# Performance work log

Measured on AMD Instinct MI355X. Metric: run time of the kernel, lower is better.

Reference implementation:

```python
import jax, jax.numpy as jnp
import numpy as np
import math

N_ANGLES = 8
HIGH_FREQ_RATIO = 0.3


def setup_inputs() -> dict:
    key = jax.random.key(0)
    k1, k2 = jax.random.split(key)
    x = jax.random.normal(k1, (4, 256, 256, 256), dtype=jnp.float32)
    # learnable per-angle weights, init near enhance_init=1.0 with small perturbation
    angle_weights = 1.0 + 0.1 * jax.random.normal(k2, (N_ANGLES,), dtype=jnp.float32)
    return {"x": x, "angle_weights": angle_weights}


def _angle_gain(H, W, angle_weights):
    # Build [H, W] real gain: angle-sector weight in the high-frequency band, 1 elsewhere.
    cy, cx = H // 2, W // 2
    y = jnp.arange(H, dtype=jnp.float32)[:, None] - cy
    x = jnp.arange(W, dtype=jnp.float32)[None, :] - cx
    r = jnp.sqrt(y * y + x * x)
    theta = jnp.arctan2(y, x) + math.pi  # [0, 2*pi]
    angle_step = 2.0 * math.pi / N_ANGLES
    angle_idx = jnp.mod(jnp.floor(theta / angle_step).astype(jnp.int32), N_ANGLES)
    r_max = min(cy, cx)
    high_freq_mask = r > HIGH_FREQ_RATIO * r_max
    weights = angle_weights[angle_idx]  # [H, W]
    return jnp.where(high_freq_mask, weights, jnp.ones_like(weights))


def reference(x, angle_weights):
    # x: [B, C, H, W]
    H, W = x.shape[-2], x.shape[-1]
    gain = _angle_gain(H, W, angle_weights)  # [H, W], real
    xf = jnp.fft.fftshift(jnp.fft.fft2(x, norm="ortho"), axes=(-2, -1))
    # mag*gain * exp(i*phase) == gain * (mag*exp(i*phase)) == gain * spectrum (gain real)
    xf_enh = xf * gain
    x_enh = jnp.fft.ifft2(jnp.fft.ifftshift(xf_enh, axes=(-2, -1)), norm="ortho").real
    return x + x_enh
```

## Files before the change

### kernel.cpp

```cpp
#include <hip/hip_runtime.h>
#include <math.h>

#define PI_F 3.14159265358979323846f
#define WSYNC() asm volatile("s_waitcnt lgkmcnt(0)" ::: "memory")

__device__ __forceinline__ float2 cmul(float2 a, float2 b) {
    return make_float2(a.x * b.x - a.y * b.y, a.x * b.y + a.y * b.x);
}
__device__ __forceinline__ float2 cmulc(float2 a, float2 b) {
    return make_float2(a.x * b.x + a.y * b.y, a.y * b.x - a.x * b.y);
}
__device__ __forceinline__ int digitrev4(int p) {
    return ((p & 3) << 6) | (((p >> 2) & 3) << 4) | (((p >> 4) & 3) << 2) | ((p >> 6) & 3);
}
__device__ __forceinline__ int SW(int i) { return i ^ ((i >> 4) & 15); }

__device__ __forceinline__ void tw3(int eu, float2& w1, float2& w2, float2& w3) {
    float sn, cs;
    __sincosf(-(2.0f * PI_F / 256.0f) * (float)eu, &sn, &cs);
    w1 = make_float2(cs, sn);
    w2 = cmul(w1, w1);
    w3 = cmul(w2, w1);
}

__device__ __forceinline__ void bfly4_fwd(float2 a0, float2 a1, float2 a2, float2 a3,
                                          float2& o0, float2& o1, float2& o2, float2& o3) {
    float2 t0 = make_float2(a0.x + a2.x, a0.y + a2.y);
    float2 t1 = make_float2(a0.x - a2.x, a0.y - a2.y);
    float2 t2 = make_float2(a1.x + a3.x, a1.y + a3.y);
    float2 u  = make_float2(a1.x - a3.x, a1.y - a3.y);
    float2 t3 = make_float2(u.y, -u.x);
    o0 = make_float2(t0.x + t2.x, t0.y + t2.y);
    o1 = make_float2(t1.x + t3.x, t1.y + t3.y);
    o2 = make_float2(t0.x - t2.x, t0.y - t2.y);
    o3 = make_float2(t1.x - t3.x, t1.y - t3.y);
}
__device__ __forceinline__ void bfly4_inv(float2 a0, float2 a1, float2 a2, float2 a3,
                                          float2& o0, float2& o1, float2& o2, float2& o3) {
    float2 t0 = make_float2(a0.x + a2.x, a0.y + a2.y);
    float2 t1 = make_float2(a0.x - a2.x, a0.y - a2.y);
    float2 t2 = make_float2(a1.x + a3.x, a1.y + a3.y);
    float2 u  = make_float2(a1.x - a3.x, a1.y - a3.y);
    float2 t3 = make_float2(-u.y, u.x);
    o0 = make_float2(t0.x + t2.x, t0.y + t2.y);
    o1 = make_float2(t1.x + t3.x, t1.y + t3.y);
    o2 = make_float2(t0.x - t2.x, t0.y - t2.y);
    o3 = make_float2(t1.x - t3.x, t1.y - t3.y);
}

template<int S>
__device__ __forceinline__ void stage_fwd_j(float2* line, int j, float2 w1, float2 w2, float2 w3) {
    const int h = 1 << (2 * S);
    int k  = j & (h - 1);
    int i0 = ((j >> (2 * S)) << (2 * S + 2)) + k;
    int p0 = SW(i0), p1 = SW(i0 + h), p2 = SW(i0 + 2 * h), p3 = SW(i0 + 3 * h);
    float2 a0 = line[p0], a1 = line[p1], a2 = line[p2], a3 = line[p3];
    float2 o0, o1, o2, o3;
    bfly4_fwd(a0, a1, a2, a3, o0, o1, o2, o3);
    line[p0] = o0;
    line[p1] = cmul(o1, w1);
    line[p2] = cmul(o2, w2);
    line[p3] = cmul(o3, w3);
}
template<int S>
__device__ __forceinline__ void stage_inv_j(float2* line, int j, float2 w1, float2 w2, float2 w3) {
    const int h = 1 << (2 * S);
    int k  = j & (h - 1);
    int i0 = ((j >> (2 * S)) << (2 * S + 2)) + k;
    int p0 = SW(i0), p1 = SW(i0 + h), p2 = SW(i0 + 2 * h), p3 = SW(i0 + 3 * h);
    float2 b0 = line[p0];
    float2 b1 = cmulc(line[p1], w1);
    float2 b2 = cmulc(line[p2], w2);
    float2 b3 = cmulc(line[p3], w3);
    float2 o0, o1, o2, o3;
    bfly4_inv(b0, b1, b2, b3, o0, o1, o2, o3);
    line[p0] = o0; line[p1] = o1; line[p2] = o2; line[p3] = o3;
}

__device__ __forceinline__ float gain1(float fy, float fx, const float* sw) {
    float r2 = fy * fy + fx * fx;
    float theta = atan2f(fy, fx) + PI_F;
    int idx = ((int)floorf(theta * (4.0f / PI_F))) & 7;
    float wv = sw[idx];
    return (r2 > 1474.56f) ? wv : 1.0f;
}

__global__ __launch_bounds__(256) void k_gain_lut(const float* __restrict__ wts, float* __restrict__ lut2) {
    __shared__ float sw[8];
    int h = threadIdx.x, w = blockIdx.x;
    if (h < 8) sw[h] = wts[h];
    __syncthreads();
    int kw = digitrev4(w), kh = digitrev4(h);
    float fx  = (kw < 128) ? (float)kw : (float)(kw - 256);
    float fx2 = (kw == 128) ? -128.0f : -fx;
    float fy  = (kh < 128) ? (float)kh : (float)(kh - 256);
    float fy2 = (kh == 128) ? -128.0f : -fy;
    float g1 = gain1(fy, fx, sw);
    float g2 = gain1(fy2, fx2, sw);
    lut2[w * 256 + h] = (1.0f + 0.5f * (g1 + g2)) * (1.0f / 65536.0f);
}

__global__ __launch_bounds__(256) void k_row_fwd(const float* __restrict__ x, float* __restrict__ out) {
    __shared__ float2 lds[8][256];
    int t = threadIdx.x, wv = t >> 6, lane = t & 63;
    int gr = blockIdx.x * 8 + wv * 2;
    int q = gr >> 8, h = gr & 255;
    int plane = ((q >> 7) << 8) + ((q & 127) << 1);
    size_t rA = ((size_t)plane << 16) + ((size_t)h << 8);
    size_t rB = rA + 65536;
    float2* L0 = lds[wv * 2];
    float2* L1 = lds[wv * 2 + 1];
    int w = lane * 4;
    float4 re0 = *(const float4*)(x + rA + w);
    float4 im0 = *(const float4*)(x + rB + w);
    float4 re1 = *(const float4*)(x + rA + 256 + w);
    float4 im1 = *(const float4*)(x + rB + 256 + w);
    float2 w31, w32, w33, w21, w22, w23, w11, w12, w13;
    tw3(lane,             w31, w32, w33);
    tw3((lane & 15) << 2, w21, w22, w23);
    tw3((lane & 3)  << 4, w11, w12, w13);
    int s0 = SW(w), s1 = SW(w + 1), s2 = SW(w + 2), s3 = SW(w + 3);
    L0[s0] = make_float2(re0.x, im0.x); L0[s1] = make_float2(re0.y, im0.y);
    L0[s2] = make_float2(re0.z, im0.z); L0[s3] = make_float2(re0.w, im0.w);
    L1[s0] = make_float2(re1.x, im1.x); L1[s1] = make_float2(re1.y, im1.y);
    L1[s2] = make_float2(re1.z, im1.z); L1[s3] = make_float2(re1.w, im1.w);
    WSYNC();
    stage_fwd_j<3>(L0, lane, w31, w32, w33); stage_fwd_j<3>(L1, lane, w31, w32, w33); WSYNC();
    stage_fwd_j<2>(L0, lane, w21, w22, w23); stage_fwd_j<2>(L1, lane, w21, w22, w23); WSYNC();
    stage_fwd_j<1>(L0, lane, w11, w12, w13); stage_fwd_j<1>(L1, lane, w11, w12, w13); WSYNC();
    {
        float2 o0, o1, o2, o3;
        bfly4_fwd(L0[s0], L0[s1], L0[s2], L0[s3], o0, o1, o2, o3);
        *(float4*)(out + rA + w) = make_float4(o0.x, o1.x, o2.x, o3.x);
        *(float4*)(out + rB + w) = make_float4(o0.y, o1.y, o2.y, o3.y);
        bfly4_fwd(L1[s0], L1[s1], L1[s2], L1[s3], o0, o1, o2, o3);
        *(float4*)(out + rA + 256 + w) = make_float4(o0.x, o1.x, o2.x, o3.x);
        *(float4*)(out + rB + 256 + w) = make_float4(o0.y, o1.y, o2.y, o3.y);
    }
}

template<bool USE_LUT>
__global__ __launch_bounds__(256) void k_col(float* __restrict__ data,
                                             const float* __restrict__ lut2,
                                             const float* __restrict__ wts) {
    __shared__ float2 tile[16][256];
    int t = threadIdx.x;
    int q = blockIdx.x >> 4, wt = blockIdx.x & 15, w0 = wt * 16;
    int plane = ((q >> 7) << 8) + ((q & 127) << 1);
    size_t baseA = ((size_t)plane << 16) + (size_t)w0;
    size_t baseB = baseA + 65536;
    int c0 = (t & 3) * 4, h0 = (t >> 2) * 4;
    int wv = t >> 6, lane = t & 63;
    int i0 = lane * 4;

    float4 gAr[2], gBr[2];
    if (!USE_LUT) {
        if (t < 8) ((float*)tile)[t] = wts[t];
        __syncthreads();
        const float* swp = (const float*)tile;
#pragma unroll
        for (int cp = 0; cp < 2; ++cp) {
#pragma unroll
            for (int cc = 0; cc < 2; ++cc) {
                int col = wv * 4 + cp * 2 + cc;
                int kw = digitrev4(w0 + col);
                float fx  = (kw < 128) ? (float)kw : (float)(kw - 256);
                float fx2 = (kw == 128) ? -128.0f : -fx;
                float4 g;
#pragma unroll
                for (int d = 0; d < 4; ++d) {
                    int kh = digitrev4(i0 + d);
                    float fy  = (kh < 128) ? (float)kh : (float)(kh - 256);
                    float fy2 = (kh == 128) ? -128.0f : -fy;
                    float g1v = gain1(fy, fx, swp);
                    float g2v = gain1(fy2, fx2, swp);
                    (&g.x)[d] = (1.0f + 0.5f * (g1v + g2v)) * (1.0f / 65536.0f);
                }
                if (cc == 0) gAr[cp] = g; else gBr[cp] = g;
            }
        }
        __syncthreads();
    }

    {
        float4 reR[4], imR[4];
#pragma unroll
        for (int r = 0; r < 4; ++r) {
            reR[r] = *(const float4*)(data + baseA + (size_t)(h0 + r) * 256 + c0);
            imR[r] = *(const float4*)(data + baseB + (size_t)(h0 + r) * 256 + c0);
        }
#pragma unroll
        for (int r = 0; r < 4; ++r) {
            int p = SW(h0 + r);
#pragma unroll
            for (int k = 0; k < 4; ++k)
                tile[c0 + k][p] = make_float2((&reR[r].x)[k], (&imR[r].x)[k]);
        }
    }
    __syncthreads();

    float2 w31, w32, w33, w21, w22, w23, w11, w12, w13;
    tw3(lane,             w31, w32, w33);
    tw3((lane & 15) << 2, w21, w22, w23);
    tw3((lane & 3)  << 4, w11, w12, w13);
    int p0 = SW(i0), p1 = SW(i0 + 1), p2 = SW(i0 + 2), p3 = SW(i0 + 3);
#pragma unroll
    for (int cp = 0; cp < 2; ++cp) {
        int colA = wv * 4 + cp * 2, colB = colA + 1;
        float2* LA = tile[colA];
        float2* LB = tile[colB];
        float4 gA, gB;
        if (USE_LUT) {
            gA = *(const float4*)(lut2 + (size_t)(w0 + colA) * 256 + i0);
            gB = *(const float4*)(lut2 + (size_t)(w0 + colB) * 256 + i0);
        } else {
            gA = gAr[cp]; gB = gBr[cp];
        }
        stage_fwd_j<3>(LA, lane, w31, w32, w33); stage_fwd_j<3>(LB, lane, w31, w32, w33); WSYNC();
        stage_fwd_j<2>(LA, lane, w21, w22, w23); stage_fwd_j<2>(LB, lane, w21, w22, w23); WSYNC();
        stage_fwd_j<1>(LA, lane, w11, w12, w13); stage_fwd_j<1>(LB, lane, w11, w12, w13); WSYNC();
        {
            float2 o0, o1, o2, o3, r0, r1, r2, r3;
            bfly4_fwd(LA[p0], LA[p1], LA[p2], LA[p3], o0, o1, o2, o3);
            o0.x *= gA.x; o0.y *= gA.x; o1.x *= gA.y; o1.y *= gA.y;
            o2.x *= gA.z; o2.y *= gA.z; o3.x *= gA.w; o3.y *= gA.w;
            bfly4_inv(o0, o1, o2, o3, r0, r1, r2, r3);
            LA[p0] = r0; LA[p1] = r1; LA[p2] = r2; LA[p3] = r3;
            bfly4_fwd(LB[p0], LB[p1], LB[p2], LB[p3], o0, o1, o2, o3);
            o0.x *= gB.x; o0.y *= gB.x; o1.x *= gB.y; o1.y *= gB.y;
            o2.x *= gB.z; o2.y *= gB.z; o3.x *= gB.w; o3.y *= gB.w;
            bfly4_inv(o0, o1, o2, o3, r0, r1, r2, r3);
            LB[p0] = r0; LB[p1] = r1; LB[p2] = r2; LB[p3] = r3;
        }
        WSYNC();
        stage_inv_j<1>(LA, lane, w11, w12, w13); stage_inv_j<1>(LB, lane, w11, w12, w13); WSYNC();
        stage_inv_j<2>(LA, lane, w21, w22, w23); stage_inv_j<2>(LB, lane, w21, w22, w23); WSYNC();
        stage_inv_j<3>(LA, lane, w31, w32, w33); stage_inv_j<3>(LB, lane, w31, w32, w33); WSYNC();
    }
    __syncthreads();

    {
#pragma unroll
        for (int r = 0; r < 4; ++r) {
            int p = SW(h0 + r);
            float2 v0 = tile[c0 + 0][p], v1 = tile[c0 + 1][p];
            float2 v2 = tile[c0 + 2][p], v3 = tile[c0 + 3][p];
            *(float4*)(data + baseA + (size_t)(h0 + r) * 256 + c0) = make_float4(v0.x, v1.x, v2.x, v3.x);
            *(float4*)(data + baseB + (size_t)(h0 + r) * 256 + c0) = make_float4(v0.y, v1.y, v2.y, v3.y);
        }
    }
}

__global__ __launch_bounds__(256) void k_row_inv(float* __restrict__ data) {
    __shared__ float2 lds[8][256];
    int t = threadIdx.x, wv = t >> 6, lane = t & 63;
    int gr = blockIdx.x * 8 + wv * 2;
    int q = gr >> 8, h = gr & 255;
    int plane = ((q >> 7) << 8) + ((q & 127) << 1);
    size_t rA = ((size_t)plane << 16) + ((size_t)h << 8);
    size_t rB = rA + 65536;
    float2* L0 = lds[wv * 2];
    float2* L1 = lds[wv * 2 + 1];
    int w = lane * 4;
    float4 re0 = *(const float4*)(data + rA + w);
    float4 im0 = *(const float4*)(data + rB + w);
    float4 re1 = *(const float4*)(data + rA + 256 + w);
    float4 im1 = *(const float4*)(data + rB + 256 + w);
    float2 w31, w32, w33, w21, w22, w23, w11, w12, w13;
    tw3(lane,             w31, w32, w33);
    tw3((lane & 15) << 2, w21, w22, w23);
    tw3((lane & 3)  << 4, w11, w12, w13);
    int s0 = SW(w), s1 = SW(w + 1), s2 = SW(w + 2), s3 = SW(w + 3);
    {
        float2 o0, o1, o2, o3;
        bfly4_inv(make_float2(re0.x, im0.x), make_float2(re0.y, im0.y),
                  make_float2(re0.z, im0.z), make_float2(re0.w, im0.w), o0, o1, o2, o3);
        L0[s0] = o0; L0[s1] = o1; L0[s2] = o2; L0[s3] = o3;
        bfly4_inv(make_float2(re1.x, im1.x), make_float2(re1.y, im1.y),
                  make_float2(re1.z, im1.z), make_float2(re1.w, im1.w), o0, o1, o2, o3);
        L1[s0] = o0; L1[s1] = o1; L1[s2] = o2; L1[s3] = o3;
    }
    WSYNC();
    stage_inv_j<1>(L0, lane, w11, w12, w13); stage_inv_j<1>(L1, lane, w11, w12, w13); WSYNC();
    stage_inv_j<2>(L0, lane, w21, w22, w23); stage_inv_j<2>(L1, lane, w21, w22, w23); WSYNC();
    stage_inv_j<3>(L0, lane, w31, w32, w33); stage_inv_j<3>(L1, lane, w31, w32, w33); WSYNC();
    float2 a0 = L0[s0], a1 = L0[s1], a2 = L0[s2], a3 = L0[s3];
    float2 b0 = L1[s0], b1 = L1[s1], b2 = L1[s2], b3 = L1[s3];
    *(float4*)(data + rA + w)       = make_float4(a0.x, a1.x, a2.x, a3.x);
    *(float4*)(data + rB + w)       = make_float4(a0.y, a1.y, a2.y, a3.y);
    *(float4*)(data + rA + 256 + w) = make_float4(b0.x, b1.x, b2.x, b3.x);
    *(float4*)(data + rB + 256 + w) = make_float4(b0.y, b1.y, b2.y, b3.y);
}

extern "C" void kernel_launch(void* const* d_in, const int* in_sizes, int n_in,
                              void* d_out, int out_size, void* d_ws, size_t ws_size,
                              hipStream_t stream) {
    const float* x   = (const float*)d_in[0];
    const float* wts = (const float*)d_in[1];
    float* out = (float*)d_out;
    (void)in_sizes; (void)n_in; (void)out_size;
    bool use_lut = (ws_size >= 256 * 256 * sizeof(float)) && (d_ws != nullptr);
    if (use_lut) {
        k_gain_lut<<<256, 256, 0, stream>>>(wts, (float*)d_ws);
    }
    k_row_fwd<<<16384, 256, 0, stream>>>(x, out);
    if (use_lut) {
        k_col<true><<<8192, 256, 0, stream>>>(out, (const float*)d_ws, wts);
    } else {
        k_col<false><<<8192, 256, 0, stream>>>(out, nullptr, wts);
    }
    k_row_inv<<<16384, 256, 0, stream>>>(out);
}
```

Before: 650.3 us.

## Replace LDS radix-4 row FFTs with register radix-2 shuffle FFT

The row forward and inverse FFT kernels drop their shared-memory radix-4 stages and instead run a decimation-in-frequency radix-2 FFT across the wavefront using __shfl_xor exchanges, finishing with a local 4-point butterfly in registers. Output ordering becomes bit-reversed rather than base-4 digit-reversed, so the gain LUT and inline gain indexing switch to bitrev8 for the row frequency axis. This removes LDS traffic and wave syncs in the row passes, at the cost of six cross-lane shuffle stages with more shuffles per element and a recurrence-based twiddle with slight precision drift.

New measurement: 653.4 us. About the same (+0.5%).

```diff
diff --git a/kernel.cpp b/kernel.cpp
--- a/kernel.cpp
+++ b/kernel.cpp
@@ -12,6 +12,9 @@
 }
 __device__ __forceinline__ int digitrev4(int p) {
     return ((p & 3) << 6) | (((p >> 2) & 3) << 4) | (((p >> 4) & 3) << 2) | ((p >> 6) & 3);
+}
+__device__ __forceinline__ int bitrev8(int p) {
+    return (int)(__brev((unsigned int)p) >> 24);
 }
 __device__ __forceinline__ int SW(int i) { return i ^ ((i >> 4) & 15); }
 
@@ -77,6 +80,69 @@
     line[p0] = o0; line[p1] = o1; line[p2] = o2; line[p3] = o3;
 }
 
+template<int MB>
+__device__ __forceinline__ void xs_fwd(float2* a, float2* b, int lane,
+                                       float step, float cC, float sC) {
+    float dm = (lane & MB) ? 1.0f : 0.0f;
+    float s  = 1.0f - 2.0f * dm;
+    float ang = step * dm * (float)(lane & (MB - 1));
+    float sn, cs; __sincosf(ang, &sn, &cs);
+    float2 tw = make_float2(cs, sn);
+    float2 Cm = make_float2(1.0f + dm * (cC - 1.0f), dm * sC);
+#pragma unroll
+    for (int d = 0; d < 4; ++d) {
+        float tax = __shfl_xor(a[d].x, MB), tay = __shfl_xor(a[d].y, MB);
+        float tbx = __shfl_xor(b[d].x, MB), tby = __shfl_xor(b[d].y, MB);
+        float2 ra = make_float2(tax + s * a[d].x, tay + s * a[d].y);
+        float2 rb = make_float2(tbx + s * b[d].x, tby + s * b[d].y);
+        a[d] = cmul(ra, tw);
+        b[d] = cmul(rb, tw);
+        tw = cmul(tw, Cm);
+    }
+}
+template<int MB>
+__device__ __forceinline__ void xs_inv(float2* a, float2* b, int lane,
+                                       float step, float cC, float sC) {
+    float dm = (lane & MB) ? 1.0f : 0.0f;
+    float s  = 1.0f - 2.0f * dm;
+    float ang = step * dm * (float)(lane & (MB - 1));
+    float sn, cs; __sincosf(ang, &sn, &cs);
+    float2 tw = make_float2(cs, sn);
+    float2 Cm = make_float2(1.0f + dm * (cC - 1.0f), dm * sC);
+#pragma unroll
+    for (int d = 0; d < 4; ++d) {
+        float2 pa = cmul(a[d], tw);
+        float2 pb = cmul(b[d], tw);
+        float tax = __shfl_xor(pa.x, MB), tay = __shfl_xor(pa.y, MB);
+        float tbx = __shfl_xor(pb.x, MB), tby = __shfl_xor(pb.y, MB);
+        a[d] = make_float2(tax + s * pa.x, tay + s * pa.y);
+        b[d] = make_float2(tbx + s * pb.x, tby + s * pb.y);
+        tw = cmul(tw, Cm);
+    }
+}
+__device__ __forceinline__ void local_fwd(float2* v) {
+    float2 u0 = make_float2(v[0].x + v[2].x, v[0].y + v[2].y);
+    float2 u2 = make_float2(v[0].x - v[2].x, v[0].y - v[2].y);
+    float2 u1 = make_float2(v[1].x + v[3].x, v[1].y + v[3].y);
+    float2 w  = make_float2(v[1].x - v[3].x, v[1].y - v[3].y);
+    float2 u3 = make_float2(w.y, -w.x);
+    v[0] = make_float2(u0.x + u1.x, u0.y + u1.y);
+    v[1] = make_float2(u0.x - u1.x, u0.y - u1.y);
+    v[2] = make_float2(u2.x + u3.x, u2.y + u3.y);
+    v[3] = make_float2(u2.x - u3.x, u2.y - u3.y);
+}
+__device__ __forceinline__ void local_inv(float2* v) {
+    float2 u0 = make_float2(v[0].x + v[1].x, v[0].y + v[1].y);
+    float2 u1 = make_float2(v[0].x - v[1].x, v[0].y - v[1].y);
+    float2 u2 = make_float2(v[2].x + v[3].x, v[2].y + v[3].y);
+    float2 u3 = make_float2(v[2].x - v[3].x, v[2].y - v[3].y);
+    float2 w  = make_float2(-u3.y, u3.x);
+    v[0] = make_float2(u0.x + u2.x, u0.y + u2.y);
+    v[2] = make_float2(u0.x - u2.x, u0.y - u2.y);
+    v[1] = make_float2(u1.x + w.x, u1.y + w.y);
+    v[3] = make_float2(u1.x - w.x, u1.y - w.y);
+}
+
 __device__ __forceinline__ float gain1(float fy, float fx, const float* sw) {
     float r2 = fy * fy + fx * fx;
     float theta = atan2f(fy, fx) + PI_F;
@@ -90,7 +156,7 @@
     int h = threadIdx.x, w = blockIdx.x;
     if (h < 8) sw[h] = wts[h];
     __syncthreads();
-    int kw = digitrev4(w), kh = digitrev4(h);
+    int kw = bitrev8(w), kh = digitrev4(h);
     float fx  = (kw < 128) ? (float)kw : (float)(kw - 256);
     float fx2 = (kw == 128) ? -128.0f : -fx;
     float fy  = (kh < 128) ? (float)kh : (float)(kh - 256);
@@ -101,42 +167,33 @@
 }
 
 __global__ __launch_bounds__(256) void k_row_fwd(const float* __restrict__ x, float* __restrict__ out) {
-    __shared__ float2 lds[8][256];
     int t = threadIdx.x, wv = t >> 6, lane = t & 63;
     int gr = blockIdx.x * 8 + wv * 2;
     int q = gr >> 8, h = gr & 255;
     int plane = ((q >> 7) << 8) + ((q & 127) << 1);
     size_t rA = ((size_t)plane << 16) + ((size_t)h << 8);
     size_t rB = rA + 65536;
-    float2* L0 = lds[wv * 2];
-    float2* L1 = lds[wv * 2 + 1];
-    int w = lane * 4;
-    float4 re0 = *(const float4*)(x + rA + w);
-    float4 im0 = *(const float4*)(x + rB + w);
-    float4 re1 = *(const float4*)(x + rA + 256 + w);
-    float4 im1 = *(const float4*)(x + rB + 256 + w);
-    float2 w31, w32, w33, w21, w22, w23, w11, w12, w13;
-    tw3(lane,             w31, w32, w33);
-    tw3((lane & 15) << 2, w21, w22, w23);
-    tw3((lane & 3)  << 4, w11, w12, w13);
-    int s0 = SW(w), s1 = SW(w + 1), s2 = SW(w + 2), s3 = SW(w + 3);
-    L0[s0] = make_float2(re0.x, im0.x); L0[s1] = make_float2(re0.y, im0.y);
-    L0[s2] = make_float2(re0.z, im0.z); L0[s3] = make_float2(re0.w, im0.w);
-    L1[s0] = make_float2(re1.x, im1.x); L1[s1] = make_float2(re1.y, im1.y);
-    L1[s2] = make_float2(re1.z, im1.z); L1[s3] = make_float2(re1.w, im1.w);
-    WSYNC();
-    stage_fwd_j<3>(L0, lane, w31, w32, w33); stage_fwd_j<3>(L1, lane, w31, w32, w33); WSYNC();
-    stage_fwd_j<2>(L0, lane, w21, w22, w23); stage_fwd_j<2>(L1, lane, w21, w22, w23); WSYNC();
-    stage_fwd_j<1>(L0, lane, w11, w12, w13); stage_fwd_j<1>(L1, lane, w11, w12, w13); WSYNC();
-    {
-        float2 o0, o1, o2, o3;
-        bfly4_fwd(L0[s0], L0[s1], L0[s2], L0[s3], o0, o1, o2, o3);
-        *(float4*)(out + rA + w) = make_float4(o0.x, o1.x, o2.x, o3.x);
-        *(float4*)(out + rB + w) = make_float4(o0.y, o1.y, o2.y, o3.y);
-        bfly4_fwd(L1[s0], L1[s1], L1[s2], L1[s3], o0, o1, o2, o3);
-        *(float4*)(out + rA + 256 + w) = make_float4(o0.x, o1.x, o2.x, o3.x);
-        *(float4*)(out + rB + 256 + w) = make_float4(o0.y, o1.y, o2.y, o3.y);
-    }
+    int w4 = lane * 4;
+    float4 re0 = *(const float4*)(x + rA + w4);
+    float4 im0 = *(const float4*)(x + rB + w4);
+    float4 re1 = *(const float4*)(x + rA + 256 + w4);
+    float4 im1 = *(const float4*)(x + rB + 256 + w4);
+    float2 a[4], b[4];
+    a[0] = make_float2(re0.x, im0.x); a[1] = make_float2(re0.y, im0.y);
+    a[2] = make_float2(re0.z, im0.z); a[3] = make_float2(re0.w, im0.w);
+    b[0] = make_float2(re1.x, im1.x); b[1] = make_float2(re1.y, im1.y);
+    b[2] = make_float2(re1.z, im1.z); b[3] = make_float2(re1.w, im1.w);
+    xs_fwd<32>(a, b, lane, -0.09817477f, 0.99969882f, -0.02454123f);
+    xs_fwd<16>(a, b, lane, -0.19634954f, 0.99879546f, -0.04906767f);
+    xs_fwd< 8>(a, b, lane, -0.39269908f, 0.99518473f, -0.09801714f);
+    xs_fwd< 4>(a, b, lane, -0.78539816f, 0.98078528f, -0.19509032f);
+    xs_fwd< 2>(a, b, lane, -1.57079633f, 0.92387953f, -0.38268343f);
+    xs_fwd< 1>(a, b, lane, -3.14159265f, 0.70710678f, -0.70710678f);
+    local_fwd(a); local_fwd(b);
+    *(float4*)(out + rA + w4)       = make_float4(a[0].x, a[1].x, a[2].x, a[3].x);
+    *(float4*)(out + rB + w4)       = make_float4(a[0].y, a[1].y, a[2].y, a[3].y);
+    *(float4*)(out + rA + 256 + w4) = make_float4(b[0].x, b[1].x, b[2].x, b[3].x);
+    *(float4*)(out + rB + 256 + w4) = make_float4(b[0].y, b[1].y, b[2].y, b[3].y);
 }
 
 template<bool USE_LUT>
@@ -163,7 +220,7 @@
 #pragma unroll
             for (int cc = 0; cc < 2; ++cc) {
                 int col = wv * 4 + cp * 2 + cc;
-                int kw = digitrev4(w0 + col);
+                int kw = bitrev8(w0 + col);
                 float fx  = (kw < 128) ? (float)kw : (float)(kw - 256);
                 float fx2 = (kw == 128) ? -128.0f : -fx;
                 float4 g;
@@ -252,44 +309,33 @@
 }
 
 __global__ __launch_bounds__(256) void k_row_inv(float* __restrict__ data) {
-    __shared__ float2 lds[8][256];
     int t = threadIdx.x, wv = t >> 6, lane = t & 63;
     int gr = blockIdx.x * 8 + wv * 2;
     int q = gr >> 8, h = gr & 255;
     int plane = ((q >> 7) << 8) + ((q & 127) << 1);
     size_t rA = ((size_t)plane << 16) + ((size_t)h << 8);
     size_t rB = rA + 65536;
-    float2* L0 = lds[wv * 2];
-    float2* L1 = lds[wv * 2 + 1];
-    int w = lane * 4;
-    float4 re0 = *(const float4*)(data + rA + w);
-    float4 im0 = *(const float4*)(data + rB + w);
-    float4 re1 = *(const float4*)(data + rA + 256 + w);
-    float4 im1 = *(const float4*)(data + rB + 256 + w);
-    float2 w31, w32, w33, w21, w22, w23, w11, w12, w13;
-    tw3(lane,             w31, w32, w33);
-    tw3((lane & 15) << 2, w21, w22, w23);
-    tw3((lane & 3)  << 4, w11, w12, w13);
-    int s0 = SW(w), s1 = SW(w + 1), s2 = SW(w + 2), s3 = SW(w + 3);
-    {
-        float2 o0, o1, o2, o3;
-        bfly4_inv(make_float2(re0.x, im0.x), make_float2(re0.y, im0.y),
-                  make_float2(re0.z, im0.z), make_float2(re0.w, im0.w), o0, o1, o2, o3);
-        L0[s0] = o0; L0[s1] = o1; L0[s2] = o2; L0[s3] = o3;
-        bfly4_inv(make_float2(re1.x, im1.x), make_float2(re1.y, im1.y),
-                  make_float2(re1.z, im1.z), make_float2(re1.w, im1.w), o0, o1, o2, o3);
-        L1[s0] = o0; L1[s1] = o1; L1[s2] = o2; L1[s3] = o3;
-    }
-    WSYNC();
-    stage_inv_j<1>(L0, lane, w11, w12, w13); stage_inv_j<1>(L1, lane, w11, w12, w13); WSYNC();
-    stage_inv_j<2>(L0, lane, w21, w22, w23); stage_inv_j<2>(L1, lane, w21, w22, w23); WSYNC();
-    stage_inv_j<3>(L0, lane, w31, w32, w33); stage_inv_j<3>(L1, lane, w31, w32, w33); WSYNC();
-    float2 a0 = L0[s0], a1 = L0[s1], a2 = L0[s2], a3 = L0[s3];
-    float2 b0 = L1[s0], b1 = L1[s1], b2 = L1[s2], b3 = L1[s3];
-    *(float4*)(data + rA + w)       = make_float4(a0.x, a1.x, a2.x, a3.x);
-    *(float4*)(data + rB + w)       = make_float4(a0.y, a1.y, a2.y, a3.y);
-    *(float4*)(data + rA + 256 + w) = make_float4(b0.x, b1.x, b2.x, b3.x);
-    *(float4*)(data + rB + 256 + w) = make_float4(b0.y, b1.y, b2.y, b3.y);
+    int w4 = lane * 4;
+    float4 re0 = *(const float4*)(data + rA + w4);
+    float4 im0 = *(const float4*)(data + rB + w4);
+    float4 re1 = *(const float4*)(data + rA + 256 + w4);
+    float4 im1 = *(const float4*)(data + rB + 256 + w4);
+    float2 a[4], b[4];
+    a[0] = make_float2(re0.x, im0.x); a[1] = make_float2(re0.y, im0.y);
+    a[2] = make_float2(re0.z, im0.z); a[3] = make_float2(re0.w, im0.w);
+    b[0] = make_float2(re1.x, im1.x); b[1] = make_float2(re1.y, im1.y);
+    b[2] = make_float2(re1.z, im1.z); b[3] = make_float2(re1.w, im1.w);
+    local_inv(a); local_inv(b);
+    xs_inv< 1>(a, b, lane,  3.14159265f, 0.70710678f,  0.70710678f);
+    xs_inv< 2>(a, b, lane,  1.57079633f, 0.92387953f,  0.38268343f);
+    xs_inv< 4>(a, b, lane,  0.78539816f, 0.98078528f,  0.19509032f);
+    xs_inv< 8>(a, b, lane,  0.39269908f, 0.99518473f,  0.09801714f);
+    xs_inv<16>(a, b, lane,  0.19634954f, 0.99879546f,  0.04906767f);
+    xs_inv<32>(a, b, lane,  0.09817477f, 0.99969882f,  0.02454123f);
+    *(float4*)(data + rA + w4)       = make_float4(a[0].x, a[1].x, a[2].x, a[3].x);
+    *(float4*)(data + rB + w4)       = make_float4(a[0].y, a[1].y, a[2].y, a[3].y);
+    *(float4*)(data + rA + 256 + w4) = make_float4(b[0].x, b[1].x, b[2].x, b[3].x);
+    *(float4*)(data + rB + 256 + w4) = make_float4(b[0].y, b[1].y, b[2].y, b[3].y);
 }
 
 extern "C" void kernel_launch(void* const* d_in, const int* in_sizes, int n_in,
```
